# Kernel optimization log

Hardware: AMD Instinct MI355X
Metric: run time of the kernel (lower is better)

## Reference

```python
import jax, jax.numpy as jnp
import numpy as np

V, N, K, D, H = 100000, 20000, 32, 256, 256


def setup_inputs() -> dict:
    key = jax.random.key(0)
    k1, k2, k3, k4, k5, k6 = jax.random.split(key, 6)
    return {
        "embed_table": jax.random.normal(k1, (V, D), dtype=jnp.float32),
        "node_ids": jax.random.randint(k2, (N,), 0, V, dtype=jnp.int64) if jax.config.jax_enable_x64 else jax.random.randint(k2, (N,), 0, V, dtype=jnp.int32),
        "nb_ids": jax.random.randint(k3, (N, K), 0, V, dtype=jnp.int32),
        "self_weight": jax.random.normal(k4, (D, H), dtype=jnp.float32) / np.sqrt(D),
        "nb_weight": jax.random.normal(k5, (D, H), dtype=jnp.float32) / np.sqrt(D),
        "bias": jax.random.normal(k6, (2 * H,), dtype=jnp.float32),
    }


def reference(embed_table, node_ids, nb_ids, self_weight, nb_weight, bias):
    # gather self embeddings: [N, D]
    self_attr = embed_table[node_ids]
    # gather sampled neighbor embeddings [N, K, D] and mean-pool over K
    nb_attr = jnp.mean(embed_table[nb_ids], axis=1)
    from_self = self_attr @ self_weight          # [N, H]
    from_nb = nb_attr @ nb_weight                # [N, H]
    out = jnp.concatenate((from_self, from_nb), axis=1) + bias  # concat combine
    return jax.nn.relu(out)
```

## Files before the change

### kernel.cpp

```cpp
#include <hip/hip_runtime.h>

#define VV 100000
#define NN 20000
#define KK 32
#define DD 256
#define HH 256
#define BN 16

#if __has_builtin(__builtin_amdgcn_global_load_lds)
#define HAS_GLL 1
#else
#define HAS_GLL 0
#endif

typedef __attribute__((ext_vector_type(8))) short bf16x8;
typedef __attribute__((ext_vector_type(4))) float f32x4;
typedef __attribute__((ext_vector_type(2))) float f32x2;
typedef __attribute__((ext_vector_type(4))) uint  u32x4;
typedef __attribute__((ext_vector_type(2))) uint  u32x2;

__device__ __forceinline__ ushort f2bf(float f) {
    uint u = __float_as_uint(f);
    return (ushort)((u + 0x7FFFu + ((u >> 16) & 1u)) >> 16);
}
__device__ __forceinline__ float bf2f(ushort u) {
    return __uint_as_float(((uint)u) << 16);
}

__global__ __launch_bounds__(256) void k_prep_all(
    const float* __restrict__ E,  unsigned char* __restrict__ E8,
    const float* __restrict__ Ws, const float* __restrict__ Wn,
    ushort* __restrict__ WT)
{
    __shared__ float t[64][65];
    const int tid = threadIdx.x;
    const int bx  = blockIdx.x;

    if (bx < 6250) {
        const size_t i = ((size_t)bx * 256 + tid) * 16;
        u32x4 o;
        #pragma unroll
        for (int w = 0; w < 4; ++w) {
            const f32x4 a = __builtin_nontemporal_load((const f32x4*)&E[i + w * 4]);
            int r = 0;
            r = __builtin_amdgcn_cvt_pk_fp8_f32(a.x, a.y, r, false);
            r = __builtin_amdgcn_cvt_pk_fp8_f32(a.z, a.w, r, true);
            o[w] = (uint)r;
        }
        *(u32x4*)&E8[i] = o;
        return;
    }

    const int pb = bx - 6250;
    const int z  = pb >> 4;
    const int rem = pb & 15;
    const int d0 = (rem & 3) * 64, h0 = (rem >> 2) * 64;
    const float* src = z ? Wn : Ws;
    ushort* dst = WT + (size_t)z * HH * DD;

    const int hl = tid & 63, dq = tid >> 6;
    #pragma unroll
    for (int i = 0; i < 16; ++i) {
        const int dl = dq * 16 + i;
        t[dl][hl] = src[(size_t)(d0 + dl) * HH + h0 + hl];
    }
    __syncthreads();
    const int dl = tid & 63, hq = tid >> 6;
    #pragma unroll
    for (int i = 0; i < 16; ++i) {
        const int h2 = hq * 16 + i;
        dst[(size_t)(h0 + h2) * DD + d0 + dl] = f2bf(t[dl][h2]);
    }
}

#if HAS_GLL
__global__ __launch_bounds__(256, 3) void k_fusedgl(
    const float*         __restrict__ Ef,
    const unsigned char* __restrict__ E8,
    const int*           __restrict__ node_ids,
    const int*           __restrict__ nb_ids,
    const ushort*        __restrict__ WT,
    const float*         __restrict__ bias,
    float*               __restrict__ out)
{
    __shared__ unsigned char stage[4][KK * 256];
    __shared__ ushort As[BN][DD];
    __shared__ ushort An[BN][DD];
    const int tid  = threadIdx.x;
    const int wv   = tid >> 6;
    const int lane = tid & 63;
    const int sub  = lane >> 5, l31 = lane & 31;
    const int g0   = blockIdx.x * BN;

    for (int it = 0; it < 4; ++it) {
        const int n = wv + it * 4;
        const int g = g0 + n;
        const int base = g * KK;

        const int srow = node_ids[g];
        const f32x4 s0 = *(const f32x4*)&Ef[(size_t)(uint)srow * DD + l31 * 8];
        const f32x4 s1 = *(const f32x4*)&Ef[(size_t)(uint)srow * DD + l31 * 8 + 4];

        #pragma unroll
        for (int j = 0; j < KK; ++j) {
            const int row = nb_ids[base + j];
            const unsigned char* gp = E8 + (size_t)(uint)row * DD + lane * 4;
            __builtin_amdgcn_global_load_lds(
                (const __attribute__((address_space(1))) void*)gp,
                (__attribute__((address_space(3))) void*)&stage[wv][j * 256],
                4, 0, 0);
        }
        asm volatile("s_waitcnt vmcnt(0)" ::: "memory");
        __builtin_amdgcn_sched_barrier(0);

        float a0 = 0.f, a1 = 0.f, a2 = 0.f, a3 = 0.f;
        #pragma unroll
        for (int j = 0; j < KK; ++j) {
            const uint w = *(const uint*)&stage[wv][j * 256 + lane * 4];
            const f32x2 lo = __builtin_amdgcn_cvt_pk_f32_fp8((int)w, false);
            const f32x2 hi = __builtin_amdgcn_cvt_pk_f32_fp8((int)w, true);
            a0 += lo.x; a1 += lo.y; a2 += hi.x; a3 += hi.y;
        }
        const float inv = 1.0f / (float)KK;
        const ushort4 nv = make_ushort4(f2bf(a0 * inv), f2bf(a1 * inv),
                                        f2bf(a2 * inv), f2bf(a3 * inv));
        const uint swz = ((uint)(n & 7)) << 4;
        *(ushort4*)((char*)&An[n][0] + ((((uint)lane) * 8) ^ swz)) = nv;
        if (sub == 0) {
            bf16x8 sv;
            sv[0] = (short)f2bf(s0.x); sv[1] = (short)f2bf(s0.y);
            sv[2] = (short)f2bf(s0.z); sv[3] = (short)f2bf(s0.w);
            sv[4] = (short)f2bf(s1.x); sv[5] = (short)f2bf(s1.y);
            sv[6] = (short)f2bf(s1.z); sv[7] = (short)f2bf(s1.w);
            *(bf16x8*)((char*)&As[n][0] + ((((uint)l31) * 16) ^ swz)) = sv;
        }
    }
    __syncthreads();

    const int half = wv >> 1;
    const int colq = (wv & 1) * 128;
    const int r16  = lane & 15;
    const int kg   = lane >> 4;
    const uint rswz = ((uint)(r16 & 7)) << 4;
    const char* Arow = (const char*)(half ? &An[r16][0] : &As[r16][0]);

    bf16x8 a[8];
    #pragma unroll
    for (int ks = 0; ks < 8; ++ks) {
        const uint off = (uint)(ks * 64 + kg * 16);
        a[ks] = *(const bf16x8*)(Arow + (off ^ rswz));
    }

    const ushort* Wb = WT + (size_t)half * HH * DD;
    f32x4 accs[8];
    #pragma unroll
    for (int ct = 0; ct < 8; ++ct) {
        const int c = colq + ct * 16 + r16;
        const ushort* Bb = Wb + (size_t)c * DD + kg * 8;
        f32x4 acc = {0.f, 0.f, 0.f, 0.f};
        #pragma unroll
        for (int ks = 0; ks < 8; ++ks) {
            const bf16x8 b = *(const bf16x8*)(Bb + ks * 32);
            acc = __builtin_amdgcn_mfma_f32_16x16x32_bf16(a[ks], b, acc, 0, 0, 0);
        }
        accs[ct] = acc;
    }

    #pragma unroll
    for (int ct = 0; ct < 8; ++ct) {
        const int cglob = half * HH + colq + ct * 16 + r16;
        const float bv = bias[cglob];
        #pragma unroll
        for (int r = 0; r < 4; ++r) {
            const float v = accs[ct][r] + bv;
            out[(size_t)(g0 + kg * 4 + r) * (2 * HH) + cglob] = v > 0.f ? v : 0.f;
        }
    }
}
#endif

__global__ __launch_bounds__(256) void k_conv8(
    const float* __restrict__ E, unsigned char* __restrict__ E8)
{
    const size_t i = ((size_t)blockIdx.x * 256 + threadIdx.x) * 16;
    u32x4 o;
    #pragma unroll
    for (int w = 0; w < 4; ++w) {
        const f32x4 a = __builtin_nontemporal_load((const f32x4*)&E[i + w * 4]);
        int r = 0;
        r = __builtin_amdgcn_cvt_pk_fp8_f32(a.x, a.y, r, false);
        r = __builtin_amdgcn_cvt_pk_fp8_f32(a.z, a.w, r, true);
        o[w] = (uint)r;
    }
    *(u32x4*)&E8[i] = o;
}

__global__ __launch_bounds__(256) void k_prep_wf(
    const float* __restrict__ Ws, const float* __restrict__ Wn,
    ushort* __restrict__ WTf)
{
    __shared__ float t[256][17];
    const int tid = threadIdx.x;
    const int h   = blockIdx.y;
    const int tt  = blockIdx.x;
    const float* src = h ? Wn : Ws;
    const int h0 = tt * 16;
    const int c = tid & 15, dr = tid >> 4;
    #pragma unroll
    for (int s = 0; s < 16; ++s) {
        const int d = s * 16 + dr;
        t[d][c] = src[(size_t)d * HH + h0 + c];
    }
    __syncthreads();
    const int fl = tid & 63, w = tid >> 6;
    const int r16 = fl & 15, kg = fl >> 4;
    #pragma unroll
    for (int p = 0; p < 2; ++p) {
        const int ks = w + p * 4;
        bf16x8 v;
        #pragma unroll
        for (int e = 0; e < 8; ++e)
            v[e] = (short)f2bf(t[ks * 32 + kg * 8 + e][r16]);
        *(bf16x8*)&WTf[(((size_t)(h * 16 + tt) * 8 + ks) * 64 + fl) * 8] = v;
    }
}

__global__ __launch_bounds__(256, 6) void k_gather8(
    const float*         __restrict__ Ef,
    const unsigned char* __restrict__ E8,
    const int*           __restrict__ node_ids,
    const int*           __restrict__ nb_ids,
    ushort*              __restrict__ A)
{
    const int wv   = threadIdx.x >> 6;
    const int lane = threadIdx.x & 63;
    const int sub  = lane >> 5, l31 = lane & 31;
    const int g    = blockIdx.x * 4 + wv;
    const int base = g * KK;

    const int srow = node_ids[g];
    const f32x4 s0 = *(const f32x4*)&Ef[(size_t)(uint)srow * DD + l31 * 8];
    const f32x4 s1 = *(const f32x4*)&Ef[(size_t)(uint)srow * DD + l31 * 8 + 4];

    u32x2 d[16];
    #pragma unroll
    for (int j = 0; j < 16; ++j) {
        const int rlo = nb_ids[base + 2 * j];
        const int rhi = nb_ids[base + 2 * j + 1];
        const int row = sub ? rhi : rlo;
        d[j] = *(const u32x2*)&E8[(size_t)(uint)row * DD + l31 * 8];
    }

    float acc[8];
    #pragma unroll
    for (int e = 0; e < 8; ++e) acc[e] = 0.f;
    #pragma unroll
    for (int j = 0; j < 16; ++j) {
        #pragma unroll
        for (int w = 0; w < 2; ++w) {
            const f32x2 lo = __builtin_amdgcn_cvt_pk_f32_fp8((int)d[j][w], false);
            const f32x2 hi = __builtin_amdgcn_cvt_pk_f32_fp8((int)d[j][w], true);
            acc[w * 4 + 0] += lo.x; acc[w * 4 + 1] += lo.y;
            acc[w * 4 + 2] += hi.x; acc[w * 4 + 3] += hi.y;
        }
    }
    #pragma unroll
    for (int e = 0; e < 8; ++e)
        acc[e] += __shfl_xor(acc[e], 32);

    const float inv = 1.0f / (float)KK;
    bf16x8 nv;
    #pragma unroll
    for (int e = 0; e < 8; ++e)
        nv[e] = (short)f2bf(acc[e] * inv);

    bf16x8 sv;
    sv[0] = (short)f2bf(s0.x); sv[1] = (short)f2bf(s0.y);
    sv[2] = (short)f2bf(s0.z); sv[3] = (short)f2bf(s0.w);
    sv[4] = (short)f2bf(s1.x); sv[5] = (short)f2bf(s1.y);
    sv[6] = (short)f2bf(s1.z); sv[7] = (short)f2bf(s1.w);

    const int tile = g >> 4, rr = g & 15;
    const int ks = l31 >> 2, kgw = l31 & 3;
    const size_t dst = (((size_t)(tile * 2 + sub) * 8 + ks) * 64 + kgw * 16 + rr) * 8;
    *(bf16x8*)&A[dst] = sub ? nv : sv;
}

__global__ __launch_bounds__(256, 4) void k_gemmf(
    const ushort* __restrict__ A,
    const ushort* __restrict__ WTf,
    const float*  __restrict__ bias,
    float*        __restrict__ out)
{
    const int wv   = __builtin_amdgcn_readfirstlane((int)(threadIdx.x >> 6));
    const int lane = threadIdx.x & 63;
    const int tile = blockIdx.x;
    const int half = wv >> 1, qt = wv & 1;
    const int r16 = lane & 15, kg = lane >> 4;

    bf16x8 a[8];
    #pragma unroll
    for (int ks = 0; ks < 8; ++ks)
        a[ks] = *(const bf16x8*)&A[(((size_t)(tile * 2 + half) * 8 + ks) * 64 + lane) * 8];

    f32x4 accs[8];
    #pragma unroll
    for (int ct = 0; ct < 8; ++ct) {
        const int t = qt * 8 + ct;
        f32x4 acc = {0.f, 0.f, 0.f, 0.f};
        #pragma unroll
        for (int ks = 0; ks < 8; ++ks) {
            const bf16x8 b = *(const bf16x8*)&WTf[(((size_t)(half * 16 + t) * 8 + ks) * 64 + lane) * 8];
            acc = __builtin_amdgcn_mfma_f32_16x16x32_bf16(a[ks], b, acc, 0, 0, 0);
        }
        accs[ct] = acc;
    }

    #pragma unroll
    for (int ct = 0; ct < 8; ++ct) {
        const int cglob = half * HH + (qt * 8 + ct) * 16 + r16;
        const float bv = bias[cglob];
        #pragma unroll
        for (int r = 0; r < 4; ++r) {
            const float v = accs[ct][r] + bv;
            out[(size_t)(tile * 16 + kg * 4 + r) * (2 * HH) + cglob] = v > 0.f ? v : 0.f;
        }
    }
}

__global__ __launch_bounds__(256, 4) void hetegraph_fused_kernel(
    const float* __restrict__ embed, const int* __restrict__ node_ids,
    const int* __restrict__ nb_ids, const float* __restrict__ Ws,
    const float* __restrict__ Wn, const float* __restrict__ bias,
    float* __restrict__ out)
{
    __shared__ float As[BN][DD];
    __shared__ float An[BN][DD];
    const int tid = threadIdx.x, wave = tid >> 6, lane = tid & 63;
    const int g0 = blockIdx.x * BN;
    for (int n = wave; n < BN; n += 4) {
        const int g = g0 + n;
        const int self_row = node_ids[g];
        const float4 s = *(const float4*)&embed[(size_t)self_row * DD + lane * 4];
        float4 acc = make_float4(0.f, 0.f, 0.f, 0.f);
        for (int k0 = 0; k0 < KK; k0 += 8) {
            float4 r[8];
            #pragma unroll
            for (int j = 0; j < 8; ++j) {
                const int row = nb_ids[g * KK + k0 + j];
                r[j] = *(const float4*)&embed[(size_t)row * DD + lane * 4];
            }
            #pragma unroll
            for (int j = 0; j < 8; ++j) {
                acc.x += r[j].x; acc.y += r[j].y; acc.z += r[j].z; acc.w += r[j].w;
            }
        }
        const float inv = 1.0f / (float)KK;
        *(float4*)&As[n][lane * 4] = s;
        float4 m = make_float4(acc.x * inv, acc.y * inv, acc.z * inv, acc.w * inv);
        *(float4*)&An[n][lane * 4] = m;
    }
    __syncthreads();
    const int h = tid;
    {
        float acc[BN];
        #pragma unroll
        for (int n = 0; n < BN; ++n) acc[n] = 0.f;
        for (int d0 = 0; d0 < DD; d0 += 4) {
            const float w0 = Ws[(d0+0)*HH+h], w1 = Ws[(d0+1)*HH+h];
            const float w2 = Ws[(d0+2)*HH+h], w3 = Ws[(d0+3)*HH+h];
            #pragma unroll
            for (int n = 0; n < BN; ++n) {
                const float4 a = *(const float4*)&As[n][d0];
                acc[n] = fmaf(a.x,w0,acc[n]); acc[n] = fmaf(a.y,w1,acc[n]);
                acc[n] = fmaf(a.z,w2,acc[n]); acc[n] = fmaf(a.w,w3,acc[n]);
            }
        }
        const float b = bias[h];
        #pragma unroll
        for (int n = 0; n < BN; ++n) {
            const float v = acc[n] + b;
            out[(size_t)(g0+n)*(2*HH) + h] = v > 0.f ? v : 0.f;
        }
    }
    {
        float acc[BN];
        #pragma unroll
        for (int n = 0; n < BN; ++n) acc[n] = 0.f;
        for (int d0 = 0; d0 < DD; d0 += 4) {
            const float w0 = Wn[(d0+0)*HH+h], w1 = Wn[(d0+1)*HH+h];
            const float w2 = Wn[(d0+2)*HH+h], w3 = Wn[(d0+3)*HH+h];
            #pragma unroll
            for (int n = 0; n < BN; ++n) {
                const float4 a = *(const float4*)&An[n][d0];
                acc[n] = fmaf(a.x,w0,acc[n]); acc[n] = fmaf(a.y,w1,acc[n]);
                acc[n] = fmaf(a.z,w2,acc[n]); acc[n] = fmaf(a.w,w3,acc[n]);
            }
        }
        const float b = bias[HH + h];
        #pragma unroll
        for (int n = 0; n < BN; ++n) {
            const float v = acc[n] + b;
            out[(size_t)(g0+n)*(2*HH) + HH + h] = v > 0.f ? v : 0.f;
        }
    }
}

extern "C" void kernel_launch(void* const* d_in, const int* in_sizes, int n_in,
                              void* d_out, int out_size, void* d_ws, size_t ws_size,
                              hipStream_t stream) {
    const float* embed    = (const float*)d_in[0];
    const int*   node_ids = (const int*)d_in[1];
    const int*   nb_ids   = (const int*)d_in[2];
    const float* Ws       = (const float*)d_in[3];
    const float* Wn       = (const float*)d_in[4];
    const float* bias     = (const float*)d_in[5];
    float*       out      = (float*)d_out;

    const size_t e8_bytes  = (size_t)VV * DD;
    const size_t wt_bytes  = 2ull * HH * DD * sizeof(ushort);
    const size_t wtf_bytes = 2ull * 16 * 8 * 64 * 8 * sizeof(ushort);
    const size_t af_bytes  = (size_t)(NN / 16) * 2 * 8 * 64 * 8 * sizeof(ushort);

#if HAS_GLL
    if (ws_size >= e8_bytes + wt_bytes) {
        unsigned char* E8 = (unsigned char*)d_ws;
        ushort*        WT = (ushort*)((char*)d_ws + e8_bytes);
        k_prep_all<<<dim3(6250 + 32), dim3(256), 0, stream>>>(embed, E8, Ws, Wn, WT);
        k_fusedgl<<<dim3(NN / BN), dim3(256), 0, stream>>>(
            embed, E8, node_ids, nb_ids, WT, bias, out);
        return;
    }
#endif
    if (ws_size >= e8_bytes + wtf_bytes + af_bytes) {
        unsigned char* E8  = (unsigned char*)d_ws;
        ushort*        WTf = (ushort*)((char*)d_ws + e8_bytes);
        ushort*        Af  = (ushort*)((char*)d_ws + e8_bytes + wtf_bytes);
        k_prep_wf<<<dim3(16, 2), dim3(256), 0, stream>>>(Ws, Wn, WTf);
        k_conv8<<<dim3(VV * DD / 4096), dim3(256), 0, stream>>>(embed, E8);
        k_gather8<<<dim3(NN / 4), dim3(256), 0, stream>>>(embed, E8, node_ids, nb_ids, Af);
        k_gemmf<<<dim3(NN / 16), dim3(256), 0, stream>>>(Af, WTf, bias, out);
    } else {
        hetegraph_fused_kernel<<<dim3(NN / BN), dim3(256), 0, stream>>>(
            embed, node_ids, nb_ids, Ws, Wn, bias, out);
    }
}
```

Before: 93.42 us.

## Double-buffer neighbor gathers in half-chunks to overlap loads with accumulation

Each wave's 32 neighbor rows are split into two 16-row halves, each with its own LDS staging buffer. The next half's global_load_lds is issued while the current half is accumulated, with a partial vmcnt wait in between. This replaces the old wait-for-all-loads-then-reduce pattern, whose per-node stall left load latency exposed. The self-embedding loads for all four nodes are also hoisted up front into registers. That costs extra VGPRs, and reusing a staging buffer right after reading it creates a possible write-after-read hazard.

After: 93.26 us. About the same (-0.2%).

```diff
diff --git a/kernel.cpp b/kernel.cpp
--- a/kernel.cpp
+++ b/kernel.cpp
@@ -83,7 +83,7 @@
     const float*         __restrict__ bias,
     float*               __restrict__ out)
 {
-    __shared__ unsigned char stage[4][KK * 256];
+    __shared__ unsigned char stage[4][2][16 * 256];
     __shared__ ushort As[BN][DD];
     __shared__ ushort An[BN][DD];
     const int tid  = threadIdx.x;
@@ -92,47 +92,68 @@
     const int sub  = lane >> 5, l31 = lane & 31;
     const int g0   = blockIdx.x * BN;
 
+    f32x4 s0[4], s1[4];
+    #pragma unroll
     for (int it = 0; it < 4; ++it) {
-        const int n = wv + it * 4;
-        const int g = g0 + n;
-        const int base = g * KK;
-
-        const int srow = node_ids[g];
-        const f32x4 s0 = *(const f32x4*)&Ef[(size_t)(uint)srow * DD + l31 * 8];
-        const f32x4 s1 = *(const f32x4*)&Ef[(size_t)(uint)srow * DD + l31 * 8 + 4];
-
-        #pragma unroll
-        for (int j = 0; j < KK; ++j) {
+        const int srow = node_ids[g0 + wv + it * 4];
+        s0[it] = *(const f32x4*)&Ef[(size_t)(uint)srow * DD + l31 * 8];
+        s1[it] = *(const f32x4*)&Ef[(size_t)(uint)srow * DD + l31 * 8 + 4];
+    }
+
+    auto issue = [&](int c) {
+        const int it = c >> 1, h = c & 1;
+        const int base = (g0 + wv + it * 4) * KK + h * 16;
+        #pragma unroll
+        for (int j = 0; j < 16; ++j) {
             const int row = nb_ids[base + j];
             const unsigned char* gp = E8 + (size_t)(uint)row * DD + lane * 4;
             __builtin_amdgcn_global_load_lds(
                 (const __attribute__((address_space(1))) void*)gp,
-                (__attribute__((address_space(3))) void*)&stage[wv][j * 256],
+                (__attribute__((address_space(3))) void*)&stage[wv][h][j * 256],
                 4, 0, 0);
         }
-        asm volatile("s_waitcnt vmcnt(0)" ::: "memory");
+    };
+
+    issue(0);
+    issue(1);
+
+    float a0 = 0.f, a1 = 0.f, a2 = 0.f, a3 = 0.f;
+    #pragma unroll
+    for (int c = 0; c < 8; ++c) {
+        if (c < 7) {
+            asm volatile("s_waitcnt vmcnt(16)" ::: "memory");
+        } else {
+            asm volatile("s_waitcnt vmcnt(0)" ::: "memory");
+        }
         __builtin_amdgcn_sched_barrier(0);
 
-        float a0 = 0.f, a1 = 0.f, a2 = 0.f, a3 = 0.f;
-        #pragma unroll
-        for (int j = 0; j < KK; ++j) {
-            const uint w = *(const uint*)&stage[wv][j * 256 + lane * 4];
+        const int h = c & 1;
+        if (h == 0) { a0 = 0.f; a1 = 0.f; a2 = 0.f; a3 = 0.f; }
+        #pragma unroll
+        for (int j = 0; j < 16; ++j) {
+            const uint w = *(const uint*)&stage[wv][h][j * 256 + lane * 4];
             const f32x2 lo = __builtin_amdgcn_cvt_pk_f32_fp8((int)w, false);
             const f32x2 hi = __builtin_amdgcn_cvt_pk_f32_fp8((int)w, true);
             a0 += lo.x; a1 += lo.y; a2 += hi.x; a3 += hi.y;
         }
-        const float inv = 1.0f / (float)KK;
-        const ushort4 nv = make_ushort4(f2bf(a0 * inv), f2bf(a1 * inv),
-                                        f2bf(a2 * inv), f2bf(a3 * inv));
-        const uint swz = ((uint)(n & 7)) << 4;
-        *(ushort4*)((char*)&An[n][0] + ((((uint)lane) * 8) ^ swz)) = nv;
-        if (sub == 0) {
-            bf16x8 sv;
-            sv[0] = (short)f2bf(s0.x); sv[1] = (short)f2bf(s0.y);
-            sv[2] = (short)f2bf(s0.z); sv[3] = (short)f2bf(s0.w);
-            sv[4] = (short)f2bf(s1.x); sv[5] = (short)f2bf(s1.y);
-            sv[6] = (short)f2bf(s1.z); sv[7] = (short)f2bf(s1.w);
-            *(bf16x8*)((char*)&As[n][0] + ((((uint)l31) * 16) ^ swz)) = sv;
+        if (c + 2 < 8) issue(c + 2);
+
+        if (h == 1) {
+            const int it = c >> 1;
+            const int n  = wv + it * 4;
+            const float inv = 1.0f / (float)KK;
+            const ushort4 nv = make_ushort4(f2bf(a0 * inv), f2bf(a1 * inv),
+                                            f2bf(a2 * inv), f2bf(a3 * inv));
+            const uint swz = ((uint)(n & 7)) << 4;
+            *(ushort4*)((char*)&An[n][0] + ((((uint)lane) * 8) ^ swz)) = nv;
+            if (sub == 0) {
+                bf16x8 sv;
+                sv[0] = (short)f2bf(s0[it].x); sv[1] = (short)f2bf(s0[it].y);
+                sv[2] = (short)f2bf(s0[it].z); sv[3] = (short)f2bf(s0[it].w);
+                sv[4] = (short)f2bf(s1[it].x); sv[5] = (short)f2bf(s1[it].y);
+                sv[6] = (short)f2bf(s1[it].z); sv[7] = (short)f2bf(s1[it].w);
+                *(bf16x8*)((char*)&As[n][0] + ((((uint)l31) * 16) ^ swz)) = sv;
+            }
         }
     }
     __syncthreads();
```
